# Optimization experiments

Hardware: AMD Instinct MI355X
Metric: run time of the kernel (lower is better)

## Reference

```python
import jax, jax.numpy as jnp
import numpy as np

N_NODES = 50000
N_EDGES = 800000
D = 64
E_DIM = 2
C = 8


def _spline_basis(pseudo, K):
    """Open B-spline basis, degree=1. pseudo: [Ne, E] in [0,1).
    Returns basis B [Ne, S] and flat weight index WI [Ne, S], S = 2**E."""
    E = pseudo.shape[1]
    v = pseudo * (K - 1)
    lo_f = jnp.floor(v)
    frac = v - lo_f
    lo = lo_f.astype(jnp.int32)
    idx = jnp.stack([jnp.clip(lo, 0, K - 1), jnp.clip(lo + 1, 0, K - 1)], axis=-1)  # [Ne,E,2]
    bas = jnp.stack([1.0 - frac, frac], axis=-1)                                   # [Ne,E,2]
    combos = jnp.asarray(
        np.stack(np.meshgrid(*([np.arange(2)] * E), indexing='ij'), -1).reshape(-1, E)
    )  # [S,E]
    d_idx = jnp.arange(E)[None, :]          # broadcast to [S,E]
    B = jnp.prod(bas[:, d_idx, combos], axis=-1)  # [Ne,S]
    stride = (K ** jnp.arange(E)).astype(jnp.int32)  # [E]
    WI = jnp.sum(idx[:, d_idx, combos] * stride[None, None, :], axis=-1)  # [Ne,S]
    return B, WI


def _spline_conv(x, src, dst, pseudo, W, root, bias, K, num_nodes):
    """SplineConv (degree=1, open spline, aggr='mean', root_weight, bias).
    x: [N,Din], W: [K**E, Din, Dout], root: [Din, Dout]."""
    B, WI = _spline_basis(pseudo, K)                 # [Ne,S], [Ne,S]
    Y = jnp.einsum('nd,kdo->nko', x, W)              # [N, K**E, Dout]
    gathered = Y[src[:, None], WI]                   # [Ne, S, Dout]
    m = jnp.einsum('es,eso->eo', B, gathered)        # [Ne, Dout]
    msum = jax.ops.segment_sum(m, dst, num_segments=num_nodes)
    cnt = jax.ops.segment_sum(jnp.ones((m.shape[0], 1), m.dtype), dst, num_segments=num_nodes)
    aggr = msum / jnp.maximum(cnt, 1.0)
    return aggr + x @ root + bias


def setup_inputs() -> dict:
    key = jax.random.key(0)
    ks = jax.random.split(key, 16)
    s = 1.0 / np.sqrt(D)
    return {
        'x': jax.random.normal(ks[0], (N_NODES, D), jnp.float32),
        'edge_index': jax.random.randint(ks[1], (2, N_EDGES), 0, N_NODES, jnp.int32),
        'edge_attr': jax.random.uniform(ks[2], (N_EDGES, E_DIM), jnp.float32),
        'W1': jax.random.normal(ks[3], (3 ** E_DIM, D, D), jnp.float32) * s,
        'root1': jax.random.normal(ks[4], (D, D), jnp.float32) * s,
        'b1': jax.random.normal(ks[5], (D,), jnp.float32) * 0.01,
        'W2': jax.random.normal(ks[6], (5 ** E_DIM, D, D), jnp.float32) * s,
        'root2': jax.random.normal(ks[7], (D, D), jnp.float32) * s,
        'b2': jax.random.normal(ks[8], (D,), jnp.float32) * 0.01,
        'mlp1_w': jax.random.normal(ks[9], (D, D), jnp.float32) * s,
        'mlp1_b': jax.random.normal(ks[10], (D,), jnp.float32) * 0.01,
        'mlp2_w': jax.random.normal(ks[11], (D, C), jnp.float32) * s,
        'mlp2_b': jax.random.normal(ks[12], (C,), jnp.float32) * 0.01,
    }


def reference(x, edge_index, edge_attr, W1, root1, b1, W2, root2, b2,
              mlp1_w, mlp1_b, mlp2_w, mlp2_b):
    N = x.shape[0]
    src, dst = edge_index[0], edge_index[1]
    h = jax.nn.elu(_spline_conv(x, src, dst, edge_attr, W1, root1, b1, 3, N))
    # dropout is identity in eval mode
    h = jax.nn.elu(_spline_conv(h, src, dst, edge_attr, W2, root2, b2, 5, N))
    # task='node', G=0 -> no pooling / no concat
    h = jax.nn.relu(h @ mlp1_w + mlp1_b)
    h = jax.nn.relu(h @ mlp2_w + mlp2_b)
    return h
```

## Files before the change

### kernel.cpp

```cpp
#include <hip/hip_runtime.h>
#include <hip/hip_bf16.h>

typedef __attribute__((ext_vector_type(8))) short short8;
typedef __attribute__((ext_vector_type(4))) float floatx4;
typedef __attribute__((ext_vector_type(16))) float floatx16;

__device__ __forceinline__ unsigned short f2bf(float x) {
  __hip_bfloat16 h = __float2bfloat16(x);
  return __builtin_bit_cast(unsigned short, h);
}
__device__ __forceinline__ float bf2f(unsigned short u) {
  return __builtin_bit_cast(float, (unsigned int)u << 16);
}

__global__ __launch_bounds__(256) void cvt_x_kernel(
    const float* __restrict__ X, unsigned short* __restrict__ Xbf, int n) {
  int i = blockIdx.x * 256 + threadIdx.x;
  if (i < n) Xbf[i] = f2bf(X[i]);
}

__global__ __launch_bounds__(256) void pack_b_kernel(
    const float* __restrict__ W, const float* __restrict__ root,
    unsigned short* __restrict__ Bpk, int K2) {
  int R = (K2 + 1) * 64;
  int total = 64 * R;
  int i = blockIdx.x * 256 + threadIdx.x;
  if (i >= total) return;
  int j = i & 7;
  int lane = (i >> 3) & 63;
  int rest = i >> 9;
  int wv = rest & 3, kc = rest >> 2;
  int o = wv * 16 + (lane & 15);
  int r = kc * 32 + ((lane >> 4) & 3) * 8 + j;
  int k = r >> 6, d = r & 63;
  float v = (k < K2) ? W[(k << 12) + (d << 6) + o] : root[(d << 6) + o];
  Bpk[i] = f2bf(v);
}

__global__ __launch_bounds__(256) void zero_int_kernel(int* __restrict__ p, int n) {
  int i = blockIdx.x * 256 + threadIdx.x;
  if (i < n) p[i] = 0;
}

__global__ __launch_bounds__(256) void hist_kernel(
    const int* __restrict__ dst, int* __restrict__ deg, int nE) {
  int e = blockIdx.x * 256 + threadIdx.x;
  if (e < nE) atomicAdd(&deg[dst[e]], 1);
}

__global__ __launch_bounds__(256) void blocksum_kernel(
    const int* __restrict__ deg, int* __restrict__ partial, int N) {
  __shared__ int s[256];
  int t = threadIdx.x, i = blockIdx.x * 256 + t;
  s[t] = (i < N) ? deg[i] : 0;
  __syncthreads();
  for (int off = 128; off > 0; off >>= 1) {
    if (t < off) s[t] += s[t + off];
    __syncthreads();
  }
  if (t == 0) partial[blockIdx.x] = s[0];
}

__global__ __launch_bounds__(256) void scanpartials_kernel(
    int* __restrict__ partial, int nb) {
  __shared__ int s[256];
  int t = threadIdx.x;
  int v = (t < nb) ? partial[t] : 0;
  s[t] = v;
  __syncthreads();
  for (int off = 1; off < 256; off <<= 1) {
    int x = (t >= off) ? s[t - off] : 0;
    __syncthreads();
    s[t] += x;
    __syncthreads();
  }
  if (t < nb) partial[t] = s[t] - v;
}

__global__ __launch_bounds__(256) void blockscan_kernel(
    const int* __restrict__ deg, const int* __restrict__ partial,
    int* __restrict__ row_start, int* __restrict__ cursor, int N, int nE) {
  __shared__ int s[256];
  int t = threadIdx.x, i = blockIdx.x * 256 + t;
  int v = (i < N) ? deg[i] : 0;
  s[t] = v;
  __syncthreads();
  for (int off = 1; off < 256; off <<= 1) {
    int x = (t >= off) ? s[t - off] : 0;
    __syncthreads();
    s[t] += x;
    __syncthreads();
  }
  if (i < N) {
    int excl = s[t] - v + partial[blockIdx.x];
    row_start[i] = excl;
    cursor[i] = excl;
  }
  if (i == 0) row_start[N] = nE;
}

__global__ __launch_bounds__(256) void scatter_rec_kernel(
    const int* __restrict__ dst, const int* __restrict__ src,
    const float* __restrict__ attr, int* __restrict__ cursor,
    float4* __restrict__ rec3, float4* __restrict__ rec5, int nE) {
  int e = blockIdx.x * 256 + threadIdx.x;
  if (e >= nE) return;
  int pos = atomicAdd(&cursor[dst[e]], 1);
  float2 a = *(const float2*)&attr[2 * e];
  int off = src[e] * 64;
  {
    float u = a.x * 2.f, v = a.y * 2.f;
    int l0 = min((int)u, 1), l1 = min((int)v, 1);
    rec3[pos] = make_float4(u - (float)l0, v - (float)l1,
                            __builtin_bit_cast(float, l0 | (l1 << 8)),
                            __builtin_bit_cast(float, off));
  }
  {
    float u = a.x * 4.f, v = a.y * 4.f;
    int l0 = min((int)u, 3), l1 = min((int)v, 3);
    rec5[pos] = make_float4(u - (float)l0, v - (float)l1,
                            __builtin_bit_cast(float, l0 | (l1 << 8)),
                            __builtin_bit_cast(float, off));
  }
}

template <int K, int K2, int OUTBF>
__global__ __launch_bounds__(256) void spline_layer_kernel(
    const float4* __restrict__ rec, const int* __restrict__ row_start,
    const unsigned short* __restrict__ Xbf, const unsigned short* __restrict__ Bpk,
    const float* __restrict__ bias, void* __restrict__ outv, int N) {
  constexpr int RZ = K2 * 64;
  constexpr int AS = RZ + 8;
  constexpr int NKZ = RZ / 32;
  constexpr int NKC = (K2 + 1) * 2;
  __shared__ unsigned short As[16 * AS];
  const int t = threadIdx.x, w = t >> 6, lane = t & 63;
  const int nodeBase = blockIdx.x * 16;

  const int col = lane & 31, half = lane >> 5;
  const int mi0 = (col < K2) ? (col % K) : -3;
  const int mi1 = (col < K2) ? (col / K) : -3;

  for (int g = 0; g < 4; ++g) {
    const int row = w * 4 + g;
    const int node = nodeBase + row;
    if (node < N) {
      floatx16 d0, d1;
#pragma unroll
      for (int i = 0; i < 16; ++i) { d0[i] = 0.f; d1[i] = 0.f; }

      const int beg = row_start[node], end = row_start[node + 1];
      for (int c0 = beg; c0 < end; c0 += 16) {
        const int m = min(16, end - c0);
        float4 rj[8];
#pragma unroll
        for (int j = 0; j < 8; ++j) {
          int idx = half * 8 + j;
          rj[j] = rec[c0 + min(idx, m - 1)];
          if (idx >= m) rj[j].z = __builtin_bit_cast(float, 0x7F7F);
        }
        short8 A, Blo, Bhi;
#pragma unroll
        for (int j = 0; j < 8; ++j) {
          int lp = __builtin_bit_cast(int, rj[j].z);
          int off = __builtin_bit_cast(int, rj[j].w);
          int l0 = lp & 0xFF, l1 = (lp >> 8) & 0xFF;
          float su = (mi0 == l0) ? (1.f - rj[j].x) : ((mi0 == l0 + 1) ? rj[j].x : 0.f);
          float sv = (mi1 == l1) ? (1.f - rj[j].y) : ((mi1 == l1 + 1) ? rj[j].y : 0.f);
          A[j] = (short)f2bf(su * sv);
          Blo[j] = (short)Xbf[off + col];
          Bhi[j] = (short)Xbf[off + 32 + col];
        }
        d0 = __builtin_amdgcn_mfma_f32_32x32x16_bf16(A, Blo, d0, 0, 0, 0);
        d1 = __builtin_amdgcn_mfma_f32_32x32x16_bf16(A, Bhi, d1, 0, 0, 0);
      }

      const float inv = 1.f / (float)max(end - beg, 1);
#pragma unroll
      for (int reg = 0; reg < 16; ++reg) {
        int r = (reg & 3) + 8 * (reg >> 2) + 4 * half;
        if (r < K2) {
          As[row * AS + r * 64 + col] = f2bf(d0[reg] * inv);
          As[row * AS + r * 64 + 32 + col] = f2bf(d1[reg] * inv);
        }
      }
    } else {
      for (int i = lane; i < RZ; i += 64) As[row * AS + i] = 0;
    }
  }
  __syncthreads();

  const int mrow = lane & 15, q = lane >> 4;
  const int anode = min(nodeBase + mrow, N - 1);
  floatx4 acc = {0.f, 0.f, 0.f, 0.f};
#pragma unroll
  for (int kc = 0; kc < NKC; ++kc) {
    short8 a;
    if (kc < NKZ)
      a = *(const short8*)&As[mrow * AS + kc * 32 + q * 8];
    else
      a = *(const short8*)&Xbf[(size_t)anode * 64 + (kc - NKZ) * 32 + q * 8];
    short8 b = *(const short8*)&Bpk[(((size_t)kc * 4 + w) * 64 + lane) * 8];
    acc = __builtin_amdgcn_mfma_f32_16x16x32_bf16(a, b, acc, 0, 0, 0);
  }

  const int o = w * 16 + mrow;
  const float bv = bias[o];
#pragma unroll
  for (int reg = 0; reg < 4; ++reg) {
    int node = nodeBase + q * 4 + reg;
    if (node < N) {
      float v = acc[reg] + bv;
      v = v > 0.f ? v : (expf(v) - 1.f);
      if (OUTBF)
        ((unsigned short*)outv)[(size_t)node * 64 + o] = f2bf(v);
      else
        ((float*)outv)[(size_t)node * 64 + o] = v;
    }
  }
}

__global__ __launch_bounds__(256) void head_kernel(
    const unsigned short* __restrict__ h2bf, const unsigned short* __restrict__ m1pk,
    const float* __restrict__ m1b, const float* __restrict__ m2w,
    const float* __restrict__ m2b, float* __restrict__ out, int N) {
  __shared__ unsigned short Hs[64 * 72];
  __shared__ unsigned short Ts[64 * 72];
  __shared__ float W2s[512];
  const int t = threadIdx.x, w = t >> 6, lane = t & 63;
  const int n0 = blockIdx.x * 64;

  for (int i = t; i < 512; i += 256) {
    int row = i >> 3, cg = i & 7;
    int n = n0 + row;
    floatx4 val = {0.f, 0.f, 0.f, 0.f};
    if (n < N) val = *(const floatx4*)&h2bf[(size_t)n * 64 + cg * 8];
    *(floatx4*)&Hs[row * 72 + cg * 8] = val;
  }
  for (int i = t; i < 512; i += 256) W2s[i] = m2w[i];
  __syncthreads();

  const int mrow = lane & 15, q = lane >> 4;
  const int o = w * 16 + mrow;
  const float bv = m1b[o];
#pragma unroll
  for (int rg = 0; rg < 4; ++rg) {
    floatx4 acc = {0.f, 0.f, 0.f, 0.f};
#pragma unroll
    for (int kc = 0; kc < 2; ++kc) {
      short8 a = *(const short8*)&Hs[(rg * 16 + mrow) * 72 + kc * 32 + q * 8];
      short8 b = *(const short8*)&m1pk[(((size_t)kc * 4 + w) * 64 + lane) * 8];
      acc = __builtin_amdgcn_mfma_f32_16x16x32_bf16(a, b, acc, 0, 0, 0);
    }
#pragma unroll
    for (int reg = 0; reg < 4; ++reg) {
      int row = rg * 16 + q * 4 + reg;
      float v = acc[reg] + bv;
      Ts[row * 72 + o] = f2bf(v > 0.f ? v : 0.f);
    }
  }
  __syncthreads();

  for (int i = t; i < 512; i += 256) {
    int nl = i >> 3, c = i & 7;
    int n = n0 + nl;
    if (n >= N) continue;
    float s = m2b[c];
    for (int d = 0; d < 64; ++d) s += bf2f(Ts[nl * 72 + d]) * W2s[d * 8 + c];
    out[(size_t)n * 8 + c] = s > 0.f ? s : 0.f;
  }
}

extern "C" void kernel_launch(void* const* d_in, const int* in_sizes, int n_in,
                              void* d_out, int out_size, void* d_ws, size_t ws_size,
                              hipStream_t stream) {
  const float* x     = (const float*)d_in[0];
  const int*   ei    = (const int*)d_in[1];
  const float* attr  = (const float*)d_in[2];
  const float* W1    = (const float*)d_in[3];
  const float* root1 = (const float*)d_in[4];
  const float* b1    = (const float*)d_in[5];
  const float* W2    = (const float*)d_in[6];
  const float* root2 = (const float*)d_in[7];
  const float* b2    = (const float*)d_in[8];
  const float* m1w   = (const float*)d_in[9];
  const float* m1b   = (const float*)d_in[10];
  const float* m2w   = (const float*)d_in[11];
  const float* m2b   = (const float*)d_in[12];

  const int N  = in_sizes[0] / 64;
  const int nE = in_sizes[1] / 2;
  const int* src  = ei;
  const int* dstv = ei + nE;
  float* out = (float*)d_out;

  int* deg       = (int*)d_ws;
  int* row_start = deg + N;
  int* cursor    = row_start + (N + 1);
  int* partial   = cursor + N;
  char* pbase = (char*)(partial + 256);
  pbase = (char*)(((uintptr_t)pbase + 15) & ~(uintptr_t)15);
  float4* rec3 = (float4*)pbase;
  float4* rec5 = rec3 + nE;
  unsigned short* Xbf  = (unsigned short*)(rec5 + nE);
  unsigned short* h1bf = Xbf + (size_t)N * 64;
  unsigned short* h2bf = h1bf + (size_t)N * 64;
  unsigned short* Bpk1 = h2bf + (size_t)N * 64;
  unsigned short* Bpk2 = Bpk1 + 64 * 640;
  unsigned short* m1pk = Bpk2 + 64 * 1664;

  dim3 blk(256);
  int nbN  = (N + 255) / 256;
  int nbE  = (nE + 255) / 256;
  int nbF  = (N + 15) / 16;
  int nbH  = (N + 63) / 64;

  zero_int_kernel<<<nbN, blk, 0, stream>>>(deg, N);
  hist_kernel<<<nbE, blk, 0, stream>>>(dstv, deg, nE);
  blocksum_kernel<<<nbN, blk, 0, stream>>>(deg, partial, N);
  scanpartials_kernel<<<1, blk, 0, stream>>>(partial, nbN);
  blockscan_kernel<<<nbN, blk, 0, stream>>>(deg, partial, row_start, cursor, N, nE);
  scatter_rec_kernel<<<nbE, blk, 0, stream>>>(dstv, src, attr, cursor, rec3, rec5, nE);

  pack_b_kernel<<<(64 * 640 + 255) / 256, blk, 0, stream>>>(W1, root1, Bpk1, 9);
  pack_b_kernel<<<(64 * 1664 + 255) / 256, blk, 0, stream>>>(W2, root2, Bpk2, 25);
  pack_b_kernel<<<(64 * 64 + 255) / 256, blk, 0, stream>>>(m1w, m1w, m1pk, 0);
  cvt_x_kernel<<<(N * 64 + 255) / 256, blk, 0, stream>>>(x, Xbf, N * 64);

  spline_layer_kernel<3, 9, 1><<<nbF, blk, 0, stream>>>(
      rec3, row_start, Xbf, Bpk1, b1, h1bf, N);

  spline_layer_kernel<5, 25, 1><<<nbF, blk, 0, stream>>>(
      rec5, row_start, h1bf, Bpk2, b2, h2bf, N);

  head_kernel<<<nbH, blk, 0, stream>>>(h2bf, m1pk, m1b, m2w, m2b, out, N);
}
```

Measured before the change: 348.1 us.

## Simplify spline basis math, pack LDS stores, shrink layer-2 tile, batch MFMA loads

Edge records now store only the scaled pseudo coordinates and the source offset. Each basis weight is computed as a hat function max(0,1-|m-u|), which replaces the index compare and select logic. The aggregated rows are written to LDS as packed 32-bit pairs, and the root/W packing is permuted so the interleaved layout still lines up. Layer 2 uses 12-node blocks to cut LDS use, and a launch-bounds hint is added to raise occupancy. The final GEMM loop loads GRP A/B fragments before issuing its MFMAs to hide load latency. The price is more blocks for layer 2, and record loads near the array end are clamped against nE.

```diff
diff --git a/kernel.cpp b/kernel.cpp
--- a/kernel.cpp
+++ b/kernel.cpp
@@ -31,8 +31,9 @@
   int rest = i >> 9;
   int wv = rest & 3, kc = rest >> 2;
   int o = wv * 16 + (lane & 15);
-  int r = kc * 32 + ((lane >> 4) & 3) * 8 + j;
-  int k = r >> 6, d = r & 63;
+  int p = kc * 32 + ((lane >> 4) & 3) * 8 + j;
+  int k = p >> 6, q6 = p & 63;
+  int d = (k < K2) ? (((q6 & 1) << 5) | (q6 >> 1)) : q6;
   float v = (k < K2) ? W[(k << 12) + (d << 6) + o] : root[(d << 6) + o];
   Bpk[i] = f2bf(v);
 }
@@ -107,42 +108,31 @@
   if (e >= nE) return;
   int pos = atomicAdd(&cursor[dst[e]], 1);
   float2 a = *(const float2*)&attr[2 * e];
-  int off = src[e] * 64;
-  {
-    float u = a.x * 2.f, v = a.y * 2.f;
-    int l0 = min((int)u, 1), l1 = min((int)v, 1);
-    rec3[pos] = make_float4(u - (float)l0, v - (float)l1,
-                            __builtin_bit_cast(float, l0 | (l1 << 8)),
-                            __builtin_bit_cast(float, off));
-  }
-  {
-    float u = a.x * 4.f, v = a.y * 4.f;
-    int l0 = min((int)u, 3), l1 = min((int)v, 3);
-    rec5[pos] = make_float4(u - (float)l0, v - (float)l1,
-                            __builtin_bit_cast(float, l0 | (l1 << 8)),
-                            __builtin_bit_cast(float, off));
-  }
-}
-
-template <int K, int K2, int OUTBF>
-__global__ __launch_bounds__(256) void spline_layer_kernel(
+  float offf = __builtin_bit_cast(float, src[e] * 64);
+  rec3[pos] = make_float4(a.x * 2.f, a.y * 2.f, offf, 0.f);
+  rec5[pos] = make_float4(a.x * 4.f, a.y * 4.f, offf, 0.f);
+}
+
+template <int K, int K2, int OUTBF, int NODES, int GRP>
+__global__ __launch_bounds__(256, 4) void spline_layer_kernel(
     const float4* __restrict__ rec, const int* __restrict__ row_start,
     const unsigned short* __restrict__ Xbf, const unsigned short* __restrict__ Bpk,
-    const float* __restrict__ bias, void* __restrict__ outv, int N) {
+    const float* __restrict__ bias, void* __restrict__ outv, int N, int nE) {
   constexpr int RZ = K2 * 64;
   constexpr int AS = RZ + 8;
   constexpr int NKZ = RZ / 32;
   constexpr int NKC = (K2 + 1) * 2;
-  __shared__ unsigned short As[16 * AS];
+  constexpr int GN = NODES / 4;
+  __shared__ unsigned short As[NODES * AS];
   const int t = threadIdx.x, w = t >> 6, lane = t & 63;
-  const int nodeBase = blockIdx.x * 16;
+  const int nodeBase = blockIdx.x * NODES;
 
   const int col = lane & 31, half = lane >> 5;
-  const int mi0 = (col < K2) ? (col % K) : -3;
-  const int mi1 = (col < K2) ? (col / K) : -3;
-
-  for (int g = 0; g < 4; ++g) {
-    const int row = w * 4 + g;
+  const float mi0f = (col < K2) ? (float)(col % K) : -1e9f;
+  const float mi1f = (col < K2) ? (float)(col / K) : 0.f;
+
+  for (int g = 0; g < GN; ++g) {
+    const int row = w * GN + g;
     const int node = nodeBase + row;
     if (node < N) {
       floatx16 d0, d1;
@@ -151,25 +141,22 @@
 
       const int beg = row_start[node], end = row_start[node + 1];
       for (int c0 = beg; c0 < end; c0 += 16) {
-        const int m = min(16, end - c0);
+        const int ib = c0 + half * 8;
         float4 rj[8];
 #pragma unroll
+        for (int j = 0; j < 8; ++j)
+          rj[j] = rec[min(ib + j, nE - 1)];
+        short8 A, Blo, Bhi;
+#pragma unroll
         for (int j = 0; j < 8; ++j) {
-          int idx = half * 8 + j;
-          rj[j] = rec[c0 + min(idx, m - 1)];
-          if (idx >= m) rj[j].z = __builtin_bit_cast(float, 0x7F7F);
-        }
-        short8 A, Blo, Bhi;
-#pragma unroll
-        for (int j = 0; j < 8; ++j) {
-          int lp = __builtin_bit_cast(int, rj[j].z);
-          int off = __builtin_bit_cast(int, rj[j].w);
-          int l0 = lp & 0xFF, l1 = (lp >> 8) & 0xFF;
-          float su = (mi0 == l0) ? (1.f - rj[j].x) : ((mi0 == l0 + 1) ? rj[j].x : 0.f);
-          float sv = (mi1 == l1) ? (1.f - rj[j].y) : ((mi1 == l1 + 1) ? rj[j].y : 0.f);
-          A[j] = (short)f2bf(su * sv);
-          Blo[j] = (short)Xbf[off + col];
-          Bhi[j] = (short)Xbf[off + 32 + col];
+          float su = fmaxf(0.f, 1.f - fabsf(mi0f - rj[j].x));
+          float sv = fmaxf(0.f, 1.f - fabsf(mi1f - rj[j].y));
+          float p = (ib + j < end) ? su * sv : 0.f;
+          A[j] = (short)f2bf(p);
+          const unsigned short* xp =
+              Xbf + __builtin_bit_cast(int, rj[j].z) + col;
+          Blo[j] = (short)xp[0];
+          Bhi[j] = (short)xp[32];
         }
         d0 = __builtin_amdgcn_mfma_f32_32x32x16_bf16(A, Blo, d0, 0, 0, 0);
         d1 = __builtin_amdgcn_mfma_f32_32x32x16_bf16(A, Bhi, d1, 0, 0, 0);
@@ -180,37 +167,47 @@
       for (int reg = 0; reg < 16; ++reg) {
         int r = (reg & 3) + 8 * (reg >> 2) + 4 * half;
         if (r < K2) {
-          As[row * AS + r * 64 + col] = f2bf(d0[reg] * inv);
-          As[row * AS + r * 64 + 32 + col] = f2bf(d1[reg] * inv);
+          unsigned int pk =
+              ((unsigned int)f2bf(d1[reg] * inv) << 16) | f2bf(d0[reg] * inv);
+          *(unsigned int*)&As[row * AS + r * 64 + col * 2] = pk;
         }
       }
     } else {
-      for (int i = lane; i < RZ; i += 64) As[row * AS + i] = 0;
+      for (int i = lane; i < RZ / 2; i += 64)
+        ((unsigned int*)&As[row * AS])[i] = 0;
     }
   }
   __syncthreads();
 
   const int mrow = lane & 15, q = lane >> 4;
-  const int anode = min(nodeBase + mrow, N - 1);
+  const int arow = (NODES < 16) ? min(mrow, NODES - 1) : mrow;
+  const int anode = min(nodeBase + arow, N - 1);
   floatx4 acc = {0.f, 0.f, 0.f, 0.f};
 #pragma unroll
-  for (int kc = 0; kc < NKC; ++kc) {
-    short8 a;
-    if (kc < NKZ)
-      a = *(const short8*)&As[mrow * AS + kc * 32 + q * 8];
-    else
-      a = *(const short8*)&Xbf[(size_t)anode * 64 + (kc - NKZ) * 32 + q * 8];
-    short8 b = *(const short8*)&Bpk[(((size_t)kc * 4 + w) * 64 + lane) * 8];
-    acc = __builtin_amdgcn_mfma_f32_16x16x32_bf16(a, b, acc, 0, 0, 0);
+  for (int kc0 = 0; kc0 < NKC; kc0 += GRP) {
+    short8 av[GRP], bv[GRP];
+#pragma unroll
+    for (int u = 0; u < GRP; ++u) {
+      const int kc = kc0 + u;
+      if (kc < NKZ)
+        av[u] = *(const short8*)&As[arow * AS + kc * 32 + q * 8];
+      else
+        av[u] = *(const short8*)&Xbf[(size_t)anode * 64 + (kc - NKZ) * 32 + q * 8];
+      bv[u] = *(const short8*)&Bpk[(((size_t)kc * 4 + w) * 64 + lane) * 8];
+    }
+#pragma unroll
+    for (int u = 0; u < GRP; ++u)
+      acc = __builtin_amdgcn_mfma_f32_16x16x32_bf16(av[u], bv[u], acc, 0, 0, 0);
   }
 
   const int o = w * 16 + mrow;
-  const float bv = bias[o];
+  const float bvs = bias[o];
 #pragma unroll
   for (int reg = 0; reg < 4; ++reg) {
-    int node = nodeBase + q * 4 + reg;
-    if (node < N) {
-      float v = acc[reg] + bv;
+    int rloc = q * 4 + reg;
+    int node = nodeBase + rloc;
+    if (rloc < NODES && node < N) {
+      float v = acc[reg] + bvs;
       v = v > 0.f ? v : (expf(v) - 1.f);
       if (OUTBF)
         ((unsigned short*)outv)[(size_t)node * 64 + o] = f2bf(v);
@@ -312,7 +309,8 @@
   dim3 blk(256);
   int nbN  = (N + 255) / 256;
   int nbE  = (nE + 255) / 256;
-  int nbF  = (N + 15) / 16;
+  int nbF1 = (N + 15) / 16;
+  int nbF2 = (N + 11) / 12;
   int nbH  = (N + 63) / 64;
 
   zero_int_kernel<<<nbN, blk, 0, stream>>>(deg, N);
@@ -327,11 +325,11 @@
   pack_b_kernel<<<(64 * 64 + 255) / 256, blk, 0, stream>>>(m1w, m1w, m1pk, 0);
   cvt_x_kernel<<<(N * 64 + 255) / 256, blk, 0, stream>>>(x, Xbf, N * 64);
 
-  spline_layer_kernel<3, 9, 1><<<nbF, blk, 0, stream>>>(
-      rec3, row_start, Xbf, Bpk1, b1, h1bf, N);
-
-  spline_layer_kernel<5, 25, 1><<<nbF, blk, 0, stream>>>(
-      rec5, row_start, h1bf, Bpk2, b2, h2bf, N);
+  spline_layer_kernel<3, 9, 1, 16, 2><<<nbF1, blk, 0, stream>>>(
+      rec3, row_start, Xbf, Bpk1, b1, h1bf, N, nE);
+
+  spline_layer_kernel<5, 25, 1, 12, 4><<<nbF2, blk, 0, stream>>>(
+      rec5, row_start, h1bf, Bpk2, b2, h2bf, N, nE);
 
   head_kernel<<<nbH, blk, 0, stream>>>(h2bf, m1pk, m1b, m2w, m2b, out, N);
 }
```

After: 319.2 us. 8.3% less time.
